# Optimization experiments

Measured on AMD Instinct MI355X. Metric: run time of the kernel, lower is better.

The kernel has to match this reference:

```python
import jax, jax.numpy as jnp
import numpy as np

B, S, N, F, E, EF, H, L = 4, 16, 2048, 32, 16384, 8, 64, 2
H2 = H // 2


def setup_inputs() -> dict:
    key = jax.random.key(0)
    ks = iter(jax.random.split(key, 40))

    def g(shape, s=0.05):
        return jax.random.normal(next(ks), shape, jnp.float32) * s

    return dict(
        x=jax.random.normal(next(ks), (B, S, N, F), jnp.float32),
        edge_index=jax.random.randint(next(ks), (2, E), 0, N, dtype=jnp.int32),
        edge_attr=jax.random.normal(next(ks), (E, EF), jnp.float32),
        Wp=g((F, H)), bp=jnp.zeros((H,), jnp.float32),
        Wl=g((L, H, H)), bl=jnp.zeros((L, H), jnp.float32),
        Wr=g((L, H, H)), br=jnp.zeros((L, H), jnp.float32),
        We=g((L, EF, H)), att=g((L, H)), gb=jnp.zeros((L, H), jnp.float32),
        Wih=g((L, 3 * H, H)), Whh=g((L, 3 * H, H)),
        bih=jnp.zeros((L, 3 * H), jnp.float32), bhh=jnp.zeros((L, 3 * H), jnp.float32),
        oW1=g((H, H2)), ob1=jnp.zeros((H2,), jnp.float32),
        oW2=g((H2, 1)), ob2=jnp.zeros((1,), jnp.float32),
        dW1=g((H, H2)), db1=jnp.zeros((H2,), jnp.float32),
        dW2=g((H2, 1)), db2=jnp.zeros((1,), jnp.float32),
    )


def reference(x, edge_index, edge_attr, Wp, bp, Wl, bl, Wr, br, We, att, gb,
              Wih, Whh, bih, bhh, oW1, ob1, oW2, ob2, dW1, db1, dW2, db2):
    b, s, n, f = x.shape
    nl, _, h = Wl.shape
    src, dst = edge_index[0], edge_index[1]
    # GATv2Conv add_self_loops with fill_value='mean': self-loop attr = mean of
    # incoming edge attrs per destination node (0 if none).
    ones = jnp.ones((src.shape[0],), x.dtype)
    cnt = jax.ops.segment_sum(ones, dst, num_segments=n)
    loop_attr = jax.ops.segment_sum(edge_attr, dst, num_segments=n) / jnp.maximum(cnt, 1.0)[:, None]
    ar = jnp.arange(n, dtype=src.dtype)
    src_f = jnp.concatenate([src, ar])
    dst_f = jnp.concatenate([dst, ar])
    ea_f = jnp.concatenate([edge_attr, loop_attr], axis=0)  # [E2, EF]

    def gat(Xg, l):
        # Xg: [G, N, H] -- GATv2 (heads=1) applied independently per graph.
        XL = Xg @ Wl[l] + bl[l]
        XR = Xg @ Wr[l] + br[l]
        ep = ea_f @ We[l]                              # [E2, H]
        m = XL[:, src_f] + XR[:, dst_f] + ep[None]     # [G, E2, H]
        m = jax.nn.leaky_relu(m, 0.2)
        logits = m @ att[l]                            # [G, E2]
        seg_max = jax.vmap(lambda lg: jax.ops.segment_max(lg, dst_f, num_segments=n))(logits)
        p = jnp.exp(logits - seg_max[:, dst_f])
        den = jax.vmap(lambda pg: jax.ops.segment_sum(pg, dst_f, num_segments=n))(p)
        alpha = p / den[:, dst_f]
        out = jax.vmap(lambda a, xl: jax.ops.segment_sum(a[:, None] * xl[src_f], dst_f, num_segments=n))(alpha, XL)
        return out + gb[l]

    def gru(seq, l):
        # seq: [T, M, H]; PyTorch GRU gate order (r, z, n), scan over T.
        def step(hprev, xt):
            gi = xt @ Wih[l].T + bih[l]
            gh = hprev @ Whh[l].T + bhh[l]
            ir, iz, inn = jnp.split(gi, 3, -1)
            hr, hz, hn = jnp.split(gh, 3, -1)
            r = jax.nn.sigmoid(ir + hr)
            z = jax.nn.sigmoid(iz + hz)
            nn_ = jnp.tanh(inn + r * hn)
            hnew = (1.0 - z) * nn_ + z * hprev
            return hnew, hnew
        h0 = jnp.zeros(seq.shape[1:], seq.dtype)
        _, ys = jax.lax.scan(step, h0, seq)
        return ys

    X = x @ Wp + bp  # [B, S, N, H]
    for l in range(nl):
        # Original code applies GAT per (outer-t, inner-b) pair; the inner
        # TemporalGNN's GRU recurs over the BATCH axis (length B) per outer t.
        hg = gat(X.reshape(b * s, n, h), l).reshape(b, s, n, h)
        X = gru(hg.reshape(b, s * n, h), l).reshape(b, s, n, h)
    xl = X[:, -1].reshape(b * n, h)  # x[:, -1] then per-node heads, concat dim=1
    order = jax.nn.relu(xl @ oW1 + ob1) @ oW2 + ob2
    demand = jax.nn.relu(xl @ dW1 + db1) @ dW2 + db2
    return order[None], demand[None]  # each [1, B*N, 1]
```

## Files before the change

kernel.cpp:

```cpp
#include <hip/hip_runtime.h>
#include <math.h>

#define Bb   4
#define Ss   16
#define Nn   2048
#define Ff   32
#define Ee   16384
#define EFf  8
#define Hh   64
#define HB2  32
#define E2c  (Ee + Nn)
#define RTOT (Bb*Ss*Nn)
#define Mm   (Ss*Nn)
#define CST  68

typedef __attribute__((ext_vector_type(8))) short short8;
typedef __attribute__((ext_vector_type(4))) float f32x4;
#define MFMA16 __builtin_amdgcn_mfma_f32_16x16x32_bf16

__device__ __forceinline__ float sigf(float x) { return 1.f / (1.f + __expf(-x)); }
__device__ __forceinline__ float tanhfast(float x) { return 2.f / (1.f + __expf(-2.f * x)) - 1.f; }

__device__ __forceinline__ void split_bf16(float x, unsigned short& h, unsigned short& l) {
  unsigned u = __float_as_uint(x);
  unsigned r = (u + 0x7FFFu + ((u >> 16) & 1u)) >> 16;
  h = (unsigned short)r;
  float rest = x - __uint_as_float(r << 16);
  unsigned u2 = __float_as_uint(rest);
  l = (unsigned short)((u2 + 0x7FFFu + ((u2 >> 16) & 1u)) >> 16);
}

template <int PAT>
__device__ __forceinline__ float xorf(float v) {
  return __int_as_float(__builtin_amdgcn_ds_swizzle(__float_as_int(v), PAT));
}
__device__ __forceinline__ float red8(float v) {
  int x = __builtin_amdgcn_update_dpp(0, __float_as_int(v), 0x128, 0xF, 0xF, true);
  v += __int_as_float(x);
  v += xorf<0x401F>(v);
  v += __shfl_xor(v, 32, 64);
  return v;
}
__device__ __forceinline__ float redlogit(float v) {
  int x;
  x = __builtin_amdgcn_update_dpp(0, __float_as_int(v), 0xB1, 0xF, 0xF, true);
  v += __int_as_float(x);
  x = __builtin_amdgcn_update_dpp(0, __float_as_int(v), 0x4E, 0xF, 0xF, true);
  v += __int_as_float(x);
  v += xorf<0x101F>(v);
  return v;
}

__global__ __launch_bounds__(256) void k_loop_accum(
    const int* __restrict__ ei, const float* __restrict__ ea,
    float* __restrict__ cntF, float* __restrict__ loopA) {
  int idx = blockIdx.x * 256 + threadIdx.x;
  int e = idx >> 3, j = idx & 7;
  int d = ei[Ee + e];
  atomicAdd(&loopA[d * EFf + j], ea[idx]);
  if (j == 0) atomicAdd(&cntF[d], 1.0f);
}

__global__ __launch_bounds__(256) void k_scan(
    const float* __restrict__ cntF, int* __restrict__ offs) {
  __shared__ int partial[256];
  int tid = threadIdx.x;
  int base = tid * 8;
  int vals[8];
  int s = 0;
  for (int i = 0; i < 8; ++i) {
    int c = (int)cntF[base + i] + 1;
    vals[i] = c;
    s += c;
  }
  partial[tid] = s;
  __syncthreads();
  for (int off = 1; off < 256; off <<= 1) {
    int v = partial[tid];
    int add = (tid >= off) ? partial[tid - off] : 0;
    __syncthreads();
    partial[tid] = v + add;
    __syncthreads();
  }
  int run = (tid == 0) ? 0 : partial[tid - 1];
  for (int i = 0; i < 8; ++i) {
    offs[base + i] = run;
    run += vals[i];
  }
  if (tid == 255) offs[Nn] = run;
}

__global__ __launch_bounds__(256) void k_scatter(
    const int* __restrict__ ei, const int* __restrict__ offs,
    int* __restrict__ fillI, int* __restrict__ posOf, int* __restrict__ srcA) {
  int e = blockIdx.x * 256 + threadIdx.x;
  if (e >= E2c) return;
  int d = (e < Ee) ? ei[Ee + e] : (e - Ee);
  int s = (e < Ee) ? ei[e]      : (e - Ee);
  int pos = offs[d] + atomicAdd(&fillI[d], 1);
  posOf[e] = pos;
  srcA[pos] = s;
}

__global__ __launch_bounds__(256) void k_wprep(
    const float* __restrict__ Wl, const float* __restrict__ Wr,
    const float* __restrict__ Wih, const float* __restrict__ Whh,
    unsigned short* __restrict__ WXhi, unsigned short* __restrict__ WXlo,
    unsigned short* __restrict__ WGhi, unsigned short* __restrict__ WGlo) {
  int idx = blockIdx.x * 256 + threadIdx.x;
  if (idx < 16384) {
    int j = idx & 7, lane = (idx >> 3) & 63, kh = (idx >> 9) & 1;
    int t = (idx >> 10) & 7, l = idx >> 13;
    int n = t * 16 + (lane & 15);
    int k = kh * 32 + ((lane >> 4) << 3) + j;
    const float* W = (n < 64) ? (Wl + (size_t)l * 4096) : (Wr + (size_t)l * 4096);
    float v = W[k * 64 + (n & 63)];
    unsigned short h, lo;
    split_bf16(v, h, lo);
    WXhi[idx] = h; WXlo[idx] = lo;
  } else {
    int i2 = idx - 16384;
    int j = i2 & 7, lane = (i2 >> 3) & 63, kh = (i2 >> 9) & 1;
    int t = (i2 >> 10) % 24, l = i2 / 24576;
    int n = t * 16 + (lane & 15);
    int k = kh * 32 + ((lane >> 4) << 3) + j;
    int g = n >> 6, c = n & 63;
    const float* W = (g < 3) ? (Wih + (size_t)l * 12288 + (size_t)(g * 64 + c) * 64)
                             : (Whh + (size_t)l * 12288 + (size_t)((g - 3) * 64 + c) * 64);
    float v = W[k];
    unsigned short h, lo;
    split_bf16(v, h, lo);
    WGhi[i2] = h; WGlo[i2] = lo;
  }
}

__global__ __launch_bounds__(256) void k_ep(
    const float* __restrict__ ea, const float* __restrict__ loopA,
    const float* __restrict__ We, const int* __restrict__ posOf,
    const float* __restrict__ cntF, float* __restrict__ EPc) {
  __shared__ float wlds[EFf * Hh];
  int tid = threadIdx.x;
  int l = blockIdx.y;
  const float* Wel = We + (size_t)l * EFf * Hh;
  if (tid < EFf * Hh) wlds[tid] = Wel[tid];
  if (tid + 256 < EFf * Hh) wlds[tid + 256] = Wel[tid + 256];
  __syncthreads();
  int idx = blockIdx.x * 256 + tid;
  int e = idx >> 6, j = idx & 63;
  const float* a = (e < Ee) ? (ea + (size_t)e * EFf) : (loopA + (size_t)(e - Ee) * EFf);
  float acc = 0.f;
#pragma unroll
  for (int k = 0; k < EFf; ++k) acc += a[k] * wlds[k * Hh + j];
  if (e >= Ee) acc /= fmaxf(cntF[e - Ee], 1.0f);
  EPc[(size_t)l * E2c * Hh + (((size_t)posOf[e]) << 6) + j] = acc;
}

__global__ __launch_bounds__(256) void k_proj(
    const float* __restrict__ X, const float* __restrict__ Wp,
    const float* __restrict__ bp, float* __restrict__ Out) {
  __shared__ float w[32 * 16];
  int tid = threadIdx.x;
  int j0 = blockIdx.y << 4;
  for (int idx = tid; idx < 32 * 16; idx += 256)
    w[idx] = Wp[((idx >> 4) << 6) + j0 + (idx & 15)];
  __syncthreads();
  int r0 = (blockIdx.x << 9) + tid;
  float acc[2][16];
#pragma unroll
  for (int jj = 0; jj < 16; ++jj) { float b = bp[j0 + jj]; acc[0][jj] = b; acc[1][jj] = b; }
  const float* x0 = X + ((size_t)r0 << 5);
  const float* x1 = x0 + (256 << 5);
  for (int kc = 0; kc < 8; ++kc) {
    float4 a0 = *(const float4*)(x0 + 4 * kc);
    float4 a1 = *(const float4*)(x1 + 4 * kc);
    float a0a[4] = {a0.x, a0.y, a0.z, a0.w};
    float a1a[4] = {a1.x, a1.y, a1.z, a1.w};
#pragma unroll
    for (int q = 0; q < 4; ++q) {
      const float4* wp4 = (const float4*)(w + ((4 * kc + q) << 4));
#pragma unroll
      for (int q4 = 0; q4 < 4; ++q4) {
        float4 wv = wp4[q4];
        acc[0][4*q4+0] = fmaf(a0a[q], wv.x, acc[0][4*q4+0]);
        acc[0][4*q4+1] = fmaf(a0a[q], wv.y, acc[0][4*q4+1]);
        acc[0][4*q4+2] = fmaf(a0a[q], wv.z, acc[0][4*q4+2]);
        acc[0][4*q4+3] = fmaf(a0a[q], wv.w, acc[0][4*q4+3]);
        acc[1][4*q4+0] = fmaf(a1a[q], wv.x, acc[1][4*q4+0]);
        acc[1][4*q4+1] = fmaf(a1a[q], wv.y, acc[1][4*q4+1]);
        acc[1][4*q4+2] = fmaf(a1a[q], wv.z, acc[1][4*q4+2]);
        acc[1][4*q4+3] = fmaf(a1a[q], wv.w, acc[1][4*q4+3]);
      }
    }
  }
#pragma unroll
  for (int rr = 0; rr < 2; ++rr) {
    float* op = Out + (((size_t)(r0 + 256 * rr)) << 6) + j0;
#pragma unroll
    for (int q4 = 0; q4 < 4; ++q4)
      *(float4*)(op + 4 * q4) = make_float4(acc[rr][4*q4], acc[rr][4*q4+1], acc[rr][4*q4+2], acc[rr][4*q4+3]);
  }
}

__global__ __launch_bounds__(256) void k_xlr_mm(
    const float* __restrict__ X,
    const unsigned short* __restrict__ WXhi, const unsigned short* __restrict__ WXlo,
    const float* __restrict__ bl_, const float* __restrict__ br_,
    float* __restrict__ XL, float* __restrict__ XR) {
  __shared__ unsigned short ahi[4096], alo[4096];
  __shared__ float cbuf[64 * CST];
  int tid = threadIdx.x, lane = tid & 63, wv = tid >> 6;
  size_t m0 = (size_t)blockIdx.x << 6;
#pragma unroll
  for (int it = 0; it < 2; ++it) {
    int task = (it << 8) + tid;
    int row = task >> 3, cOct = task & 7;
    const float* src = X + ((m0 + row) << 6) + (cOct << 3);
    float4 a = *(const float4*)src;
    float4 b = *(const float4*)(src + 4);
    float va[8] = {a.x, a.y, a.z, a.w, b.x, b.y, b.z, b.w};
    short8 hv, lv;
#pragma unroll
    for (int j = 0; j < 8; ++j) {
      unsigned short hs, ls;
      split_bf16(va[j], hs, ls);
      hv[j] = (short)hs; lv[j] = (short)ls;
    }
    int f = ((cOct >> 2) * 4 + (row >> 4)) * 64 + ((cOct & 3) << 4) + (row & 15);
    *(short8*)&ahi[f << 3] = hv;
    *(short8*)&alo[f << 3] = lv;
  }
  __syncthreads();
  short8 Ah0 = *(const short8*)&ahi[((0 + wv) << 6 | lane) << 3];
  short8 Al0 = *(const short8*)&alo[((0 + wv) << 6 | lane) << 3];
  short8 Ah1 = *(const short8*)&ahi[((4 + wv) << 6 | lane) << 3];
  short8 Al1 = *(const short8*)&alo[((4 + wv) << 6 | lane) << 3];
  int nl = lane & 15;
  f32x4 acc[8];
#pragma unroll
  for (int t = 0; t < 8; ++t) {
    int n = t * 16 + nl;
    float b = (n < 64) ? bl_[n] : br_[n - 64];
    acc[t] = (f32x4){b, b, b, b};
  }
#pragma unroll
  for (int t = 0; t < 8; ++t) {
    const short8* bh0p = (const short8*)(WXhi + ((t << 1) << 9)) + lane;
    const short8* bl0p = (const short8*)(WXlo + ((t << 1) << 9)) + lane;
    const short8* bh1p = (const short8*)(WXhi + (((t << 1) + 1) << 9)) + lane;
    const short8* bl1p = (const short8*)(WXlo + (((t << 1) + 1) << 9)) + lane;
    short8 bh0 = *bh0p, bl0 = *bl0p, bh1 = *bh1p, bl1 = *bl1p;
    acc[t] = MFMA16(Ah0, bh0, acc[t], 0, 0, 0);
    acc[t] = MFMA16(Ah0, bl0, acc[t], 0, 0, 0);
    acc[t] = MFMA16(Al0, bh0, acc[t], 0, 0, 0);
    acc[t] = MFMA16(Ah1, bh1, acc[t], 0, 0, 0);
    acc[t] = MFMA16(Ah1, bl1, acc[t], 0, 0, 0);
    acc[t] = MFMA16(Al1, bh1, acc[t], 0, 0, 0);
  }
  int rbase = (wv << 4) + ((lane >> 4) << 2);
#pragma unroll
  for (int half = 0; half < 2; ++half) {
    __syncthreads();
#pragma unroll
    for (int tt = 0; tt < 4; ++tt) {
      int t = (half << 2) + tt;
#pragma unroll
      for (int reg = 0; reg < 4; ++reg)
        cbuf[(rbase + reg) * CST + (tt << 4) + nl] = acc[t][reg];
    }
    __syncthreads();
    float* dst = half ? XR : XL;
#pragma unroll
    for (int i = 0; i < 4; ++i) {
      int idx = (i << 10) + (tid << 2);
      int row = idx >> 6, col = idx & 63;
      *(float4*)(dst + ((m0 + row) << 6) + col) = *(float4*)&cbuf[row * CST + col];
    }
  }
}

__global__ __launch_bounds__(256) void k_gat(
    const float* __restrict__ XL, float* __restrict__ XR_HG,
    const float* __restrict__ EPc, const int* __restrict__ offs,
    const int* __restrict__ srcA,
    const float* __restrict__ att, const float* __restrict__ gbl) {
  int d = blockIdx.x;
  int q = blockIdx.y;
  int tid = threadIdx.x;
  int wv = tid >> 6, lane = tid & 63;
  int eSub = lane >> 3, hOct = lane & 7;
  int hb = hOct << 3;
  float at[8], gv[8];
  {
    float4 a0 = *(const float4*)(att + hb);
    float4 a1 = *(const float4*)(att + hb + 4);
    float4 g0v = *(const float4*)(gbl + hb);
    float4 g1v = *(const float4*)(gbl + hb + 4);
    at[0]=a0.x; at[1]=a0.y; at[2]=a0.z; at[3]=a0.w;
    at[4]=a1.x; at[5]=a1.y; at[6]=a1.z; at[7]=a1.w;
    gv[0]=g0v.x; gv[1]=g0v.y; gv[2]=g0v.z; gv[3]=g0v.w;
    gv[4]=g1v.x; gv[5]=g1v.y; gv[6]=g1v.z; gv[7]=g1v.w;
  }
  int p0 = offs[d], p1 = offs[d + 1];
  int nE = p1 - p0;
  int nCh = (nE + 7) >> 3;
  int gbase = (q << 4) + wv;
  size_t rowg[4];
  const float* Xg[4];
  float xr[4][8];
#pragma unroll
  for (int c = 0; c < 4; ++c) {
    int g = gbase + (c << 2);
    rowg[c] = ((size_t)(g * Nn + d)) << 6;
    Xg[c] = XL + (((size_t)g * Nn) << 6);
    float4 a = *(const float4*)(XR_HG + rowg[c] + hb);
    float4 b = *(const float4*)(XR_HG + rowg[c] + hb + 4);
    xr[c][0]=a.x; xr[c][1]=a.y; xr[c][2]=a.z; xr[c][3]=a.w;
    xr[c][4]=b.x; xr[c][5]=b.y; xr[c][6]=b.z; xr[c][7]=b.w;
  }
  float Sd[4] = {0.f, 0.f, 0.f, 0.f};
  float acc[4][8];
#pragma unroll
  for (int c = 0; c < 4; ++c)
#pragma unroll
    for (int j = 0; j < 8; ++j) acc[c][j] = 0.f;

  for (int ck = 0; ck < nCh; ++ck) {
    int p = (ck << 3) + eSub;
    int pc = p < nE ? p : nE - 1;
    int s = srcA[p0 + pc];
    const float* epp = EPc + (((size_t)(p0 + pc)) << 6) + hb;
    float4 e0 = *(const float4*)epp;
    float4 e1 = *(const float4*)(epp + 4);
    float ep[8] = {e0.x, e0.y, e0.z, e0.w, e1.x, e1.y, e1.z, e1.w};
    float xlv[4][8];
#pragma unroll
    for (int c = 0; c < 4; ++c) {
      const float* xp = Xg[c] + ((size_t)s << 6) + hb;
      float4 x0 = *(const float4*)xp;
      float4 x1 = *(const float4*)(xp + 4);
      xlv[c][0]=x0.x; xlv[c][1]=x0.y; xlv[c][2]=x0.z; xlv[c][3]=x0.w;
      xlv[c][4]=x1.x; xlv[c][5]=x1.y; xlv[c][6]=x1.z; xlv[c][7]=x1.w;
    }
    float v[4] = {0.f, 0.f, 0.f, 0.f};
#pragma unroll
    for (int c = 0; c < 4; ++c)
#pragma unroll
      for (int j = 0; j < 8; ++j) {
        float m = xlv[c][j] + xr[c][j] + ep[j];
        m = fmaxf(m, 0.2f * m);
        v[c] = fmaf(m, at[j], v[c]);
      }
#pragma unroll
    for (int c = 0; c < 4; ++c) v[c] = redlogit(v[c]);
    bool live = (p < nE);
#pragma unroll
    for (int c = 0; c < 4; ++c) {
      float w = live ? __expf(v[c]) : 0.f;
      Sd[c] += w;
#pragma unroll
      for (int j = 0; j < 8; ++j) acc[c][j] = fmaf(w, xlv[c][j], acc[c][j]);
    }
  }
#pragma unroll
  for (int c = 0; c < 4; ++c) {
    Sd[c] = red8(Sd[c]);
#pragma unroll
    for (int j = 0; j < 8; ++j) acc[c][j] = red8(acc[c][j]);
  }
  if (eSub == 0) {
#pragma unroll
    for (int c = 0; c < 4; ++c) {
      float inv = 1.f / Sd[c];
      float* op = XR_HG + rowg[c] + hb;
      *(float4*)(op)     = make_float4(fmaf(acc[c][0], inv, gv[0]), fmaf(acc[c][1], inv, gv[1]),
                                       fmaf(acc[c][2], inv, gv[2]), fmaf(acc[c][3], inv, gv[3]));
      *(float4*)(op + 4) = make_float4(fmaf(acc[c][4], inv, gv[4]), fmaf(acc[c][5], inv, gv[5]),
                                       fmaf(acc[c][6], inv, gv[6]), fmaf(acc[c][7], inv, gv[7]));
    }
  }
}

__device__ __forceinline__ void mm6(f32x4& acc,
    short8 Ah0, short8 Al0, short8 Ah1, short8 Al1,
    const unsigned short* __restrict__ Whi, const unsigned short* __restrict__ Wlo,
    int tt, int lane) {
  const short8* bh0p = (const short8*)(Whi + (tt << 10)) + lane;
  const short8* bl0p = (const short8*)(Wlo + (tt << 10)) + lane;
  const short8* bh1p = (const short8*)(Whi + (tt << 10) + 512) + lane;
  const short8* bl1p = (const short8*)(Wlo + (tt << 10) + 512) + lane;
  short8 bh0 = *bh0p, bl0 = *bl0p, bh1 = *bh1p, bl1 = *bl1p;
  acc = MFMA16(Ah0, bh0, acc, 0, 0, 0);
  acc = MFMA16(Ah0, bl0, acc, 0, 0, 0);
  acc = MFMA16(Al0, bh0, acc, 0, 0, 0);
  acc = MFMA16(Ah1, bh1, acc, 0, 0, 0);
  acc = MFMA16(Ah1, bl1, acc, 0, 0, 0);
  acc = MFMA16(Al1, bh1, acc, 0, 0, 0);
}

__global__ __launch_bounds__(128) void k_gru_fused(
    const float* __restrict__ hgAll,
    const unsigned short* __restrict__ WGhi, const unsigned short* __restrict__ WGlo,
    const float* __restrict__ bih, const float* __restrict__ bhh,
    float* __restrict__ houtAll) {
  __shared__ unsigned short ghi[2048], glo[2048], phi[2048], plo[2048];
  __shared__ float cbuf[32 * CST];
  int tid = threadIdx.x, lane = tid & 63, wv = tid >> 6;
  int nl = lane & 15;
  int rbase = (wv << 4) + ((lane >> 4) << 2);
  size_t m0 = (size_t)blockIdx.x << 5;

  float biasR[4], biasZ[4], biasN[4], biasH[4];
#pragma unroll
  for (int ct = 0; ct < 4; ++ct) {
    int c = (ct << 4) + nl;
    biasR[ct] = bih[c]       + bhh[c];
    biasZ[ct] = bih[64 + c]  + bhh[64 + c];
    biasN[ct] = bih[128 + c];
    biasH[ct] = bhh[128 + c];
  }
  float hreg[4][4];
#pragma unroll
  for (int ct = 0; ct < 4; ++ct)
#pragma unroll
    for (int r = 0; r < 4; ++r) hreg[ct][r] = 0.f;

  float4 pa[2], pb[2];
#pragma unroll
  for (int it = 0; it < 2; ++it) {
    int task = (it << 7) + tid;
    int row = task >> 3, cOct = task & 7;
    const float* srcg = hgAll + ((m0 + row) << 6) + (cOct << 3);
    pa[it] = *(const float4*)srcg;
    pb[it] = *(const float4*)(srcg + 4);
  }

  for (int t = 0; t < Bb; ++t) {
#pragma unroll
    for (int it = 0; it < 2; ++it) {
      int task = (it << 7) + tid;
      int row = task >> 3, cOct = task & 7;
      float va[8] = {pa[it].x, pa[it].y, pa[it].z, pa[it].w,
                     pb[it].x, pb[it].y, pb[it].z, pb[it].w};
      short8 hv8, lv8;
#pragma unroll
      for (int j = 0; j < 8; ++j) {
        unsigned short hs, ls;
        split_bf16(va[j], hs, ls);
        hv8[j] = (short)hs; lv8[j] = (short)ls;
      }
      int f = ((cOct >> 2) * 2 + (row >> 4)) * 64 + ((cOct & 3) << 4) + (row & 15);
      *(short8*)&ghi[f << 3] = hv8;
      *(short8*)&glo[f << 3] = lv8;
    }
    __syncthreads();

    short8 Gh0 = *(const short8*)&ghi[((0 + wv) << 6 | lane) << 3];
    short8 Gl0 = *(const short8*)&glo[((0 + wv) << 6 | lane) << 3];
    short8 Gh1 = *(const short8*)&ghi[((2 + wv) << 6 | lane) << 3];
    short8 Gl1 = *(const short8*)&glo[((2 + wv) << 6 | lane) << 3];

    if (t + 1 < Bb) {
      const float* hg = hgAll + (size_t)(t + 1) * ((size_t)Mm * Hh);
#pragma unroll
      for (int it = 0; it < 2; ++it) {
        int task = (it << 7) + tid;
        int row = task >> 3, cOct = task & 7;
        const float* srcg = hg + ((m0 + row) << 6) + (cOct << 3);
        pa[it] = *(const float4*)srcg;
        pb[it] = *(const float4*)(srcg + 4);
      }
    }

    f32x4 accR[4], accZ[4], accN[4], accH[4];
#pragma unroll
    for (int ct = 0; ct < 4; ++ct) {
      accR[ct] = (f32x4){biasR[ct], biasR[ct], biasR[ct], biasR[ct]};
      accZ[ct] = (f32x4){biasZ[ct], biasZ[ct], biasZ[ct], biasZ[ct]};
      accN[ct] = (f32x4){biasN[ct], biasN[ct], biasN[ct], biasN[ct]};
      accH[ct] = (f32x4){biasH[ct], biasH[ct], biasH[ct], biasH[ct]};
    }
#pragma unroll
    for (int ct = 0; ct < 4; ++ct) {
      mm6(accR[ct], Gh0, Gl0, Gh1, Gl1, WGhi, WGlo, 0 + ct, lane);
      mm6(accZ[ct], Gh0, Gl0, Gh1, Gl1, WGhi, WGlo, 4 + ct, lane);
      mm6(accN[ct], Gh0, Gl0, Gh1, Gl1, WGhi, WGlo, 8 + ct, lane);
    }
    if (t) {
      short8 Ph0 = *(const short8*)&phi[((0 + wv) << 6 | lane) << 3];
      short8 Pl0 = *(const short8*)&plo[((0 + wv) << 6 | lane) << 3];
      short8 Ph1 = *(const short8*)&phi[((2 + wv) << 6 | lane) << 3];
      short8 Pl1 = *(const short8*)&plo[((2 + wv) << 6 | lane) << 3];
#pragma unroll
      for (int ct = 0; ct < 4; ++ct) {
        mm6(accR[ct], Ph0, Pl0, Ph1, Pl1, WGhi, WGlo, 12 + ct, lane);
        mm6(accZ[ct], Ph0, Pl0, Ph1, Pl1, WGhi, WGlo, 16 + ct, lane);
        mm6(accH[ct], Ph0, Pl0, Ph1, Pl1, WGhi, WGlo, 20 + ct, lane);
      }
    }

#pragma unroll
    for (int ct = 0; ct < 4; ++ct) {
#pragma unroll
      for (int r = 0; r < 4; ++r) {
        float rg = sigf(accR[ct][r]);
        float zg = sigf(accZ[ct][r]);
        float ng = tanhfast(accN[ct][r] + rg * accH[ct][r]);
        float h = (1.f - zg) * ng + zg * hreg[ct][r];
        hreg[ct][r] = h;
        cbuf[(rbase + r) * CST + (ct << 4) + nl] = h;
      }
    }
    __syncthreads();

    float* hout = houtAll + (size_t)t * ((size_t)Mm * Hh);
#pragma unroll
    for (int i = 0; i < 4; ++i) {
      int idx = (i << 9) + (tid << 2);
      int row = idx >> 6, col = idx & 63;
      *(float4*)(hout + ((m0 + row) << 6) + col) = *(float4*)&cbuf[row * CST + col];
    }
    if (t + 1 < Bb) {
#pragma unroll
      for (int it = 0; it < 2; ++it) {
        int task = (it << 7) + tid;
        int row = task >> 3, cOct = task & 7;
        float4 q0 = *(const float4*)&cbuf[row * CST + (cOct << 3)];
        float4 q1 = *(const float4*)&cbuf[row * CST + (cOct << 3) + 4];
        float va[8] = {q0.x, q0.y, q0.z, q0.w, q1.x, q1.y, q1.z, q1.w};
        short8 hv8, lv8;
#pragma unroll
        for (int j = 0; j < 8; ++j) {
          unsigned short hs, ls;
          split_bf16(va[j], hs, ls);
          hv8[j] = (short)hs; lv8[j] = (short)ls;
        }
        int f = ((cOct >> 2) * 2 + (row >> 4)) * 64 + ((cOct & 3) << 4) + (row & 15);
        *(short8*)&phi[f << 3] = hv8;
        *(short8*)&plo[f << 3] = lv8;
      }
    }
  }
}

__global__ __launch_bounds__(256) void k_heads(
    const float* __restrict__ Xb,
    const float* __restrict__ oW1, const float* __restrict__ ob1,
    const float* __restrict__ oW2, const float* __restrict__ ob2,
    const float* __restrict__ dW1, const float* __restrict__ db1,
    const float* __restrict__ dW2, const float* __restrict__ db2,
    float* __restrict__ out) {
  __shared__ float xa[64 * 65];
  __shared__ float w1o[64 * 32], w1d[64 * 32];
  __shared__ float po[4][64], pd[4][64];
  int tid = threadIdx.x;
  int rblk = blockIdx.x << 6;
  int b = rblk >> 11;
  int n0 = rblk & (Nn - 1);
  const float* src = Xb + (((size_t)b * Ss + (Ss - 1)) * Nn + n0) * Hh;
#pragma unroll
  for (int i = 0; i < 4; ++i) {
    int idx = (i << 10) + (tid << 2);
    int row = idx >> 6, col = idx & 63;
    float4 v = *(const float4*)(src + idx);
    float* dp = &xa[row * 65 + col];
    dp[0] = v.x; dp[1] = v.y; dp[2] = v.z; dp[3] = v.w;
  }
  for (int idx = tid; idx < 2048; idx += 256) {
    w1o[idx] = oW1[idx];
    w1d[idx] = dW1[idx];
  }
  __syncthreads();
  int row = tid & 63;
  int jg = tid >> 6;
  int j0 = jg << 3;
  float hO[8], hD[8];
#pragma unroll
  for (int j = 0; j < 8; ++j) { hO[j] = ob1[j0 + j]; hD[j] = db1[j0 + j]; }
  const float* xr = &xa[row * 65];
  for (int k = 0; k < 64; ++k) {
    float xv = xr[k];
    const float4* wo = (const float4*)&w1o[(k << 5) + j0];
    const float4* wd = (const float4*)&w1d[(k << 5) + j0];
    float4 o0 = wo[0], o1 = wo[1], d0 = wd[0], d1 = wd[1];
    hO[0] = fmaf(xv, o0.x, hO[0]); hO[1] = fmaf(xv, o0.y, hO[1]);
    hO[2] = fmaf(xv, o0.z, hO[2]); hO[3] = fmaf(xv, o0.w, hO[3]);
    hO[4] = fmaf(xv, o1.x, hO[4]); hO[5] = fmaf(xv, o1.y, hO[5]);
    hO[6] = fmaf(xv, o1.z, hO[6]); hO[7] = fmaf(xv, o1.w, hO[7]);
    hD[0] = fmaf(xv, d0.x, hD[0]); hD[1] = fmaf(xv, d0.y, hD[1]);
    hD[2] = fmaf(xv, d0.z, hD[2]); hD[3] = fmaf(xv, d0.w, hD[3]);
    hD[4] = fmaf(xv, d1.x, hD[4]); hD[5] = fmaf(xv, d1.y, hD[5]);
    hD[6] = fmaf(xv, d1.z, hD[6]); hD[7] = fmaf(xv, d1.w, hD[7]);
  }
  float accoP = 0.f, accdP = 0.f;
#pragma unroll
  for (int j = 0; j < 8; ++j) {
    accoP = fmaf(fmaxf(hO[j], 0.f), oW2[j0 + j], accoP);
    accdP = fmaf(fmaxf(hD[j], 0.f), dW2[j0 + j], accdP);
  }
  po[jg][row] = accoP;
  pd[jg][row] = accdP;
  __syncthreads();
  if (tid < 64) {
    int r = rblk + tid;
    out[r]           = ob2[0] + ((po[0][tid] + po[1][tid]) + (po[2][tid] + po[3][tid]));
    out[Bb * Nn + r] = db2[0] + ((pd[0][tid] + pd[1][tid]) + (pd[2][tid] + pd[3][tid]));
  }
}

extern "C" void kernel_launch(void* const* d_in, const int* in_sizes, int n_in,
                              void* d_out, int out_size, void* d_ws, size_t ws_size,
                              hipStream_t stream) {
  const float* x   = (const float*)d_in[0];
  const int*   ei  = (const int*)d_in[1];
  const float* ea  = (const float*)d_in[2];
  const float* Wp  = (const float*)d_in[3];
  const float* bp  = (const float*)d_in[4];
  const float* Wl  = (const float*)d_in[5];
  const float* bl  = (const float*)d_in[6];
  const float* Wr  = (const float*)d_in[7];
  const float* br  = (const float*)d_in[8];
  const float* We  = (const float*)d_in[9];
  const float* att = (const float*)d_in[10];
  const float* gb  = (const float*)d_in[11];
  const float* Wih = (const float*)d_in[12];
  const float* Whh = (const float*)d_in[13];
  const float* bih = (const float*)d_in[14];
  const float* bhh = (const float*)d_in[15];
  const float* oW1 = (const float*)d_in[16];
  const float* ob1 = (const float*)d_in[17];
  const float* oW2 = (const float*)d_in[18];
  const float* ob2 = (const float*)d_in[19];
  const float* dW1 = (const float*)d_in[20];
  const float* db1 = (const float*)d_in[21];
  const float* dW2 = (const float*)d_in[22];
  const float* db2 = (const float*)d_in[23];
  float* out = (float*)d_out;

  float* f    = (float*)d_ws;
  float* Xb   = f;
  float* XLb  = Xb  + (size_t)RTOT * Hh;
  float* XRb  = XLb + (size_t)RTOT * Hh;
  float* EPc  = XRb + (size_t)RTOT * Hh;
  unsigned short* WXhi = (unsigned short*)(EPc + (size_t)2 * E2c * Hh);
  unsigned short* WXlo = WXhi + 16384;
  unsigned short* WGhi = WXlo + 16384;
  unsigned short* WGlo = WGhi + 49152;
  float* cntF = (float*)(WGlo + 49152);
  float* loopA = cntF + Nn;
  int*   fillI = (int*)(loopA + Nn * EFf);
  int*   offs  = fillI + Nn;
  int*   posOf = offs + 2052;
  int*   srcA  = posOf + E2c;

  hipMemsetAsync(cntF, 0, (size_t)(Nn + Nn * EFf + Nn) * 4, stream);

  k_loop_accum<<<dim3(Ee * EFf / 256), 256, 0, stream>>>(ei, ea, cntF, loopA);
  k_scan<<<1, 256, 0, stream>>>(cntF, offs);
  k_scatter<<<dim3((E2c + 255) / 256), 256, 0, stream>>>(ei, offs, fillI, posOf, srcA);
  k_wprep<<<dim3(256), 256, 0, stream>>>(Wl, Wr, Wih, Whh, WXhi, WXlo, WGhi, WGlo);

  k_proj<<<dim3(RTOT / 512, 4), 256, 0, stream>>>(x, Wp, bp, Xb);

  k_ep<<<dim3(E2c * Hh / 256, 2), 256, 0, stream>>>(ea, loopA, We, posOf, cntF, EPc);

  for (int l = 0; l < 2; ++l) {
    k_xlr_mm<<<dim3(RTOT / 64), 256, 0, stream>>>(
        Xb, WXhi + (size_t)l * 8192, WXlo + (size_t)l * 8192,
        bl + (size_t)l * Hh, br + (size_t)l * Hh, XLb, XRb);
    k_gat<<<dim3(Nn, 4), 256, 0, stream>>>(
        XLb, XRb, EPc + (size_t)l * E2c * Hh, offs, srcA,
        att + (size_t)l * Hh, gb + (size_t)l * Hh);
    k_gru_fused<<<dim3(Mm / 32), 128, 0, stream>>>(
        XRb, WGhi + (size_t)l * 24576, WGlo + (size_t)l * 24576,
        bih + (size_t)l * 192, bhh + (size_t)l * 192, Xb);
  }

  k_heads<<<dim3(Bb * Nn / 64), 256, 0, stream>>>(
      Xb, oW1, ob1, oW2, ob2, dW1, db1, dW2, db2, out);
}
```

Before: 444.9 us.

## Use one wavefront per GRU block covering two row tiles to reuse weight fragments

The GRU kernel now runs one 64-lane wavefront per 32-row block instead of two wavefronts, and each wave computes both 16-row tiles. Each loaded weight fragment then feeds two MFMA chains, which halves global/L2 weight loads per row. The previous hidden state is read back from LDS instead of registers, and biases are staged in LDS and added after accumulation, to hold down register pressure. The cost is half as many waves per block and more serial MFMA work per wave, which may reduce latency hiding. There are also extra LDS reads and writes per timestep.

Result: slower. 515.5 us (+15.9%).

```diff
diff --git a/kernel.cpp b/kernel.cpp
--- a/kernel.cpp
+++ b/kernel.cpp
@@ -380,54 +380,52 @@
   }
 }
 
-__device__ __forceinline__ void mm6(f32x4& acc,
+__device__ __forceinline__ void mmtile(f32x4& a0, f32x4& a1,
     short8 Ah0, short8 Al0, short8 Ah1, short8 Al1,
+    short8 Bh0, short8 Bl0, short8 Bh1, short8 Bl1,
     const unsigned short* __restrict__ Whi, const unsigned short* __restrict__ Wlo,
     int tt, int lane) {
-  const short8* bh0p = (const short8*)(Whi + (tt << 10)) + lane;
-  const short8* bl0p = (const short8*)(Wlo + (tt << 10)) + lane;
-  const short8* bh1p = (const short8*)(Whi + (tt << 10) + 512) + lane;
-  const short8* bl1p = (const short8*)(Wlo + (tt << 10) + 512) + lane;
-  short8 bh0 = *bh0p, bl0 = *bl0p, bh1 = *bh1p, bl1 = *bl1p;
-  acc = MFMA16(Ah0, bh0, acc, 0, 0, 0);
-  acc = MFMA16(Ah0, bl0, acc, 0, 0, 0);
-  acc = MFMA16(Al0, bh0, acc, 0, 0, 0);
-  acc = MFMA16(Ah1, bh1, acc, 0, 0, 0);
-  acc = MFMA16(Ah1, bl1, acc, 0, 0, 0);
-  acc = MFMA16(Al1, bh1, acc, 0, 0, 0);
-}
-
-__global__ __launch_bounds__(128) void k_gru_fused(
+  const short8* wh0p = (const short8*)(Whi + (tt << 10)) + lane;
+  const short8* wl0p = (const short8*)(Wlo + (tt << 10)) + lane;
+  const short8* wh1p = (const short8*)(Whi + (tt << 10) + 512) + lane;
+  const short8* wl1p = (const short8*)(Wlo + (tt << 10) + 512) + lane;
+  short8 h0 = *wh0p, l0 = *wl0p, h1 = *wh1p, l1 = *wl1p;
+  a0 = MFMA16(Ah0, h0, a0, 0, 0, 0);
+  a0 = MFMA16(Ah0, l0, a0, 0, 0, 0);
+  a0 = MFMA16(Al0, h0, a0, 0, 0, 0);
+  a0 = MFMA16(Ah1, h1, a0, 0, 0, 0);
+  a0 = MFMA16(Ah1, l1, a0, 0, 0, 0);
+  a0 = MFMA16(Al1, h1, a0, 0, 0, 0);
+  a1 = MFMA16(Bh0, h0, a1, 0, 0, 0);
+  a1 = MFMA16(Bh0, l0, a1, 0, 0, 0);
+  a1 = MFMA16(Bl0, h0, a1, 0, 0, 0);
+  a1 = MFMA16(Bh1, h1, a1, 0, 0, 0);
+  a1 = MFMA16(Bh1, l1, a1, 0, 0, 0);
+  a1 = MFMA16(Bl1, h1, a1, 0, 0, 0);
+}
+
+__global__ __launch_bounds__(64, 1) void k_gru_fused(
     const float* __restrict__ hgAll,
     const unsigned short* __restrict__ WGhi, const unsigned short* __restrict__ WGlo,
     const float* __restrict__ bih, const float* __restrict__ bhh,
     float* __restrict__ houtAll) {
   __shared__ unsigned short ghi[2048], glo[2048], phi[2048], plo[2048];
   __shared__ float cbuf[32 * CST];
-  int tid = threadIdx.x, lane = tid & 63, wv = tid >> 6;
+  __shared__ float blds[4 * 64];
+  int lane = threadIdx.x;
   int nl = lane & 15;
-  int rbase = (wv << 4) + ((lane >> 4) << 2);
+  int rb0 = (lane >> 4) << 2;
   size_t m0 = (size_t)blockIdx.x << 5;
 
-  float biasR[4], biasZ[4], biasN[4], biasH[4];
-#pragma unroll
-  for (int ct = 0; ct < 4; ++ct) {
-    int c = (ct << 4) + nl;
-    biasR[ct] = bih[c]       + bhh[c];
-    biasZ[ct] = bih[64 + c]  + bhh[64 + c];
-    biasN[ct] = bih[128 + c];
-    biasH[ct] = bhh[128 + c];
-  }
-  float hreg[4][4];
-#pragma unroll
-  for (int ct = 0; ct < 4; ++ct)
-#pragma unroll
-    for (int r = 0; r < 4; ++r) hreg[ct][r] = 0.f;
-
-  float4 pa[2], pb[2];
-#pragma unroll
-  for (int it = 0; it < 2; ++it) {
-    int task = (it << 7) + tid;
+  blds[lane]       = bih[lane]       + bhh[lane];
+  blds[64 + lane]  = bih[64 + lane]  + bhh[64 + lane];
+  blds[128 + lane] = bih[128 + lane];
+  blds[192 + lane] = bhh[128 + lane];
+
+  float4 pa[4], pb[4];
+#pragma unroll
+  for (int it = 0; it < 4; ++it) {
+    int task = (it << 6) + lane;
     int row = task >> 3, cOct = task & 7;
     const float* srcg = hgAll + ((m0 + row) << 6) + (cOct << 3);
     pa[it] = *(const float4*)srcg;
@@ -436,8 +434,8 @@
 
   for (int t = 0; t < Bb; ++t) {
 #pragma unroll
-    for (int it = 0; it < 2; ++it) {
-      int task = (it << 7) + tid;
+    for (int it = 0; it < 4; ++it) {
+      int task = (it << 6) + lane;
       int row = task >> 3, cOct = task & 7;
       float va[8] = {pa[it].x, pa[it].y, pa[it].z, pa[it].w,
                      pb[it].x, pb[it].y, pb[it].z, pb[it].w};
@@ -454,16 +452,20 @@
     }
     __syncthreads();
 
-    short8 Gh0 = *(const short8*)&ghi[((0 + wv) << 6 | lane) << 3];
-    short8 Gl0 = *(const short8*)&glo[((0 + wv) << 6 | lane) << 3];
-    short8 Gh1 = *(const short8*)&ghi[((2 + wv) << 6 | lane) << 3];
-    short8 Gl1 = *(const short8*)&glo[((2 + wv) << 6 | lane) << 3];
+    short8 GAh0 = *(const short8*)&ghi[((0 << 6) | lane) << 3];
+    short8 GAl0 = *(const short8*)&glo[((0 << 6) | lane) << 3];
+    short8 GAh1 = *(const short8*)&ghi[((2 << 6) | lane) << 3];
+    short8 GAl1 = *(const short8*)&glo[((2 << 6) | lane) << 3];
+    short8 GBh0 = *(const short8*)&ghi[((1 << 6) | lane) << 3];
+    short8 GBl0 = *(const short8*)&glo[((1 << 6) | lane) << 3];
+    short8 GBh1 = *(const short8*)&ghi[((3 << 6) | lane) << 3];
+    short8 GBl1 = *(const short8*)&glo[((3 << 6) | lane) << 3];
 
     if (t + 1 < Bb) {
       const float* hg = hgAll + (size_t)(t + 1) * ((size_t)Mm * Hh);
 #pragma unroll
-      for (int it = 0; it < 2; ++it) {
-        int task = (it << 7) + tid;
+      for (int it = 0; it < 4; ++it) {
+        int task = (it << 6) + lane;
         int row = task >> 3, cOct = task & 7;
         const float* srcg = hg + ((m0 + row) << 6) + (cOct << 3);
         pa[it] = *(const float4*)srcg;
@@ -471,58 +473,81 @@
       }
     }
 
-    f32x4 accR[4], accZ[4], accN[4], accH[4];
+    f32x4 accR[4][2], accZ[4][2], accN[4][2], accH[4][2];
 #pragma unroll
     for (int ct = 0; ct < 4; ++ct) {
-      accR[ct] = (f32x4){biasR[ct], biasR[ct], biasR[ct], biasR[ct]};
-      accZ[ct] = (f32x4){biasZ[ct], biasZ[ct], biasZ[ct], biasZ[ct]};
-      accN[ct] = (f32x4){biasN[ct], biasN[ct], biasN[ct], biasN[ct]};
-      accH[ct] = (f32x4){biasH[ct], biasH[ct], biasH[ct], biasH[ct]};
+      accR[ct][0] = (f32x4){0.f, 0.f, 0.f, 0.f}; accR[ct][1] = (f32x4){0.f, 0.f, 0.f, 0.f};
+      accZ[ct][0] = (f32x4){0.f, 0.f, 0.f, 0.f}; accZ[ct][1] = (f32x4){0.f, 0.f, 0.f, 0.f};
+      accN[ct][0] = (f32x4){0.f, 0.f, 0.f, 0.f}; accN[ct][1] = (f32x4){0.f, 0.f, 0.f, 0.f};
+      accH[ct][0] = (f32x4){0.f, 0.f, 0.f, 0.f}; accH[ct][1] = (f32x4){0.f, 0.f, 0.f, 0.f};
     }
 #pragma unroll
     for (int ct = 0; ct < 4; ++ct) {
-      mm6(accR[ct], Gh0, Gl0, Gh1, Gl1, WGhi, WGlo, 0 + ct, lane);
-      mm6(accZ[ct], Gh0, Gl0, Gh1, Gl1, WGhi, WGlo, 4 + ct, lane);
-      mm6(accN[ct], Gh0, Gl0, Gh1, Gl1, WGhi, WGlo, 8 + ct, lane);
+      mmtile(accR[ct][0], accR[ct][1], GAh0, GAl0, GAh1, GAl1,
+             GBh0, GBl0, GBh1, GBl1, WGhi, WGlo, 0 + ct, lane);
+      mmtile(accZ[ct][0], accZ[ct][1], GAh0, GAl0, GAh1, GAl1,
+             GBh0, GBl0, GBh1, GBl1, WGhi, WGlo, 4 + ct, lane);
+      mmtile(accN[ct][0], accN[ct][1], GAh0, GAl0, GAh1, GAl1,
+             GBh0, GBl0, GBh1, GBl1, WGhi, WGlo, 8 + ct, lane);
     }
     if (t) {
-      short8 Ph0 = *(const short8*)&phi[((0 + wv) << 6 | lane) << 3];
-      short8 Pl0 = *(const short8*)&plo[((0 + wv) << 6 | lane) << 3];
-      short8 Ph1 = *(const short8*)&phi[((2 + wv) << 6 | lane) << 3];
-      short8 Pl1 = *(const short8*)&plo[((2 + wv) << 6 | lane) << 3];
+      short8 PAh0 = *(const short8*)&phi[((0 << 6) | lane) << 3];
+      short8 PAl0 = *(const short8*)&plo[((0 << 6) | lane) << 3];
+      short8 PAh1 = *(const short8*)&phi[((2 << 6) | lane) << 3];
+      short8 PAl1 = *(const short8*)&plo[((2 << 6) | lane) << 3];
+      short8 PBh0 = *(const short8*)&phi[((1 << 6) | lane) << 3];
+      short8 PBl0 = *(const short8*)&plo[((1 << 6) | lane) << 3];
+      short8 PBh1 = *(const short8*)&phi[((3 << 6) | lane) << 3];
+      short8 PBl1 = *(const short8*)&plo[((3 << 6) | lane) << 3];
 #pragma unroll
       for (int ct = 0; ct < 4; ++ct) {
-        mm6(accR[ct], Ph0, Pl0, Ph1, Pl1, WGhi, WGlo, 12 + ct, lane);
-        mm6(accZ[ct], Ph0, Pl0, Ph1, Pl1, WGhi, WGlo, 16 + ct, lane);
-        mm6(accH[ct], Ph0, Pl0, Ph1, Pl1, WGhi, WGlo, 20 + ct, lane);
+        mmtile(accR[ct][0], accR[ct][1], PAh0, PAl0, PAh1, PAl1,
+               PBh0, PBl0, PBh1, PBl1, WGhi, WGlo, 12 + ct, lane);
+        mmtile(accZ[ct][0], accZ[ct][1], PAh0, PAl0, PAh1, PAl1,
+               PBh0, PBl0, PBh1, PBl1, WGhi, WGlo, 16 + ct, lane);
+        mmtile(accH[ct][0], accH[ct][1], PAh0, PAl0, PAh1, PAl1,
+               PBh0, PBl0, PBh1, PBl1, WGhi, WGlo, 20 + ct, lane);
       }
     }
 
-#pragma unroll
-    for (int ct = 0; ct < 4; ++ct) {
-#pragma unroll
-      for (int r = 0; r < 4; ++r) {
-        float rg = sigf(accR[ct][r]);
-        float zg = sigf(accZ[ct][r]);
-        float ng = tanhfast(accN[ct][r] + rg * accH[ct][r]);
-        float h = (1.f - zg) * ng + zg * hreg[ct][r];
-        hreg[ct][r] = h;
-        cbuf[(rbase + r) * CST + (ct << 4) + nl] = h;
+    {
+      float bR[4], bZ[4], bN[4], bH[4];
+#pragma unroll
+      for (int ct = 0; ct < 4; ++ct) {
+        int c = (ct << 4) + nl;
+        bR[ct] = blds[c]; bZ[ct] = blds[64 + c];
+        bN[ct] = blds[128 + c]; bH[ct] = blds[192 + c];
       }
+#pragma unroll
+      for (int rg = 0; rg < 2; ++rg) {
+        int rbase = (rg << 4) + rb0;
+#pragma unroll
+        for (int ct = 0; ct < 4; ++ct) {
+#pragma unroll
+          for (int r = 0; r < 4; ++r) {
+            float rgate = sigf(accR[ct][rg][r] + bR[ct]);
+            float zg = sigf(accZ[ct][rg][r] + bZ[ct]);
+            float ng = tanhfast(accN[ct][rg][r] + bN[ct] + rgate * (accH[ct][rg][r] + bH[ct]));
+            int ci = (rbase + r) * CST + (ct << 4) + nl;
+            float hp = t ? cbuf[ci] : 0.f;
+            cbuf[ci] = (1.f - zg) * ng + zg * hp;
+          }
+        }
+      }
     }
     __syncthreads();
 
     float* hout = houtAll + (size_t)t * ((size_t)Mm * Hh);
 #pragma unroll
-    for (int i = 0; i < 4; ++i) {
-      int idx = (i << 9) + (tid << 2);
+    for (int i = 0; i < 8; ++i) {
+      int idx = (i << 8) + (lane << 2);
       int row = idx >> 6, col = idx & 63;
       *(float4*)(hout + ((m0 + row) << 6) + col) = *(float4*)&cbuf[row * CST + col];
     }
     if (t + 1 < Bb) {
 #pragma unroll
-      for (int it = 0; it < 2; ++it) {
-        int task = (it << 7) + tid;
+      for (int it = 0; it < 4; ++it) {
+        int task = (it << 6) + lane;
         int row = task >> 3, cOct = task & 7;
         float4 q0 = *(const float4*)&cbuf[row * CST + (cOct << 3)];
         float4 q1 = *(const float4*)&cbuf[row * CST + (cOct << 3) + 4];
@@ -670,7 +695,7 @@
     k_gat<<<dim3(Nn, 4), 256, 0, stream>>>(
         XLb, XRb, EPc + (size_t)l * E2c * Hh, offs, srcA,
         att + (size_t)l * Hh, gb + (size_t)l * Hh);
-    k_gru_fused<<<dim3(Mm / 32), 128, 0, stream>>>(
+    k_gru_fused<<<dim3(Mm / 32), 64, 0, stream>>>(
         XRb, WGhi + (size_t)l * 24576, WGlo + (size_t)l * 24576,
         bih + (size_t)l * 192, bhh + (size_t)l * 192, Xb);
   }
```
